# Kernel tuning notes

Hardware: AMD Instinct MI355X
Metric: run time of the kernel (lower is better)

## Reference

```python
import jax, jax.numpy as jnp
import numpy as np

TAGSET = 50
START_TAG = 48
END_TAG = 49
SEQ_LEN = 512
BATCH = 64
HIDDEN = 512


def setup_inputs() -> dict:
    key = jax.random.key(0)
    k1, k2, k3, k4 = jax.random.split(key, 4)
    feats = jax.random.normal(k1, (SEQ_LEN, BATCH, HIDDEN), dtype=jnp.float32)
    W = jax.random.normal(k2, (TAGSET * TAGSET, HIDDEN), dtype=jnp.float32) * (1.0 / np.sqrt(HIDDEN))
    b = jax.random.normal(k3, (TAGSET * TAGSET,), dtype=jnp.float32) * 0.01
    target = jax.random.randint(k4, (SEQ_LEN, BATCH, 1), 0, TAGSET * TAGSET, dtype=jnp.int64)
    mask = jnp.ones((SEQ_LEN, BATCH), dtype=bool)
    return {"feats": feats, "W": W, "b": b, "target": target, "mask": mask}


def reference(feats, W, b, target, mask):
    S, B, H = feats.shape
    T = TAGSET
    # hidden2tag: Linear(H -> T*T), then view (S, B, T_from, T_to)
    scores = jnp.einsum('sbh,kh->sbk', feats, W) + b  # (S, B, T*T)
    scores4 = scores.reshape(S, B, T, T)

    # gold-path energy: gather flattened (from,to) index per position, mask, sum
    tg_energy = jnp.take_along_axis(scores, target, axis=2)[..., 0]  # (S, B)
    tg_sum = jnp.sum(jnp.where(mask, tg_energy, jnp.zeros((), scores.dtype)))

    # forward algorithm (log-sum-exp semiring scan over time)
    partition0 = scores4[0, :, START_TAG, :]  # (B, T)

    def step(partition, xs):
        cur, m = xs  # cur: (B, T_from, T_to), m: (B,)
        new = jax.nn.logsumexp(cur + partition[:, :, None], axis=1)  # (B, T)
        partition = jnp.where(m[:, None], new, partition)
        return partition, None

    partition, _ = jax.lax.scan(step, partition0, (scores4[1:], mask[1:]))
    loss = (jnp.sum(partition[:, END_TAG]) - tg_sum) / B
    return loss
```

## Files before the change

### kernel.cpp

```cpp
#include <hip/hip_runtime.h>
#include <math.h>


#define KK    2500
#define KPAD  2560
#define NROW  32768
#define MTS   72
#define MTS2  80
#define ARS   144
#define LN2   0.69314718055994530942f
#define LOG2E 1.44269504088896340736f

typedef __attribute__((ext_vector_type(8))) short short8;
typedef __attribute__((ext_vector_type(8))) unsigned short ushort8;
typedef __attribute__((ext_vector_type(4))) float f32x4;
typedef __attribute__((ext_vector_type(4))) int int4v;
typedef __attribute__((ext_vector_type(8))) int int8v;
typedef __attribute__((ext_vector_type(2))) unsigned int uint2v;

__device__ __forceinline__ unsigned short f2bf(float f){
  unsigned int u = __builtin_bit_cast(unsigned int, f);
  u += 0x7fffu + ((u >> 16) & 1u);
  return (unsigned short)(u >> 16);
}
__device__ __forceinline__ float bf2f(unsigned short h){
  return __builtin_bit_cast(float, ((unsigned int)h) << 16);
}
__device__ __forceinline__ unsigned int pk_fp8x4(float a0, float a1, float a2, float a3){
  unsigned int p = __builtin_amdgcn_cvt_pk_fp8_f32(a0, a1, 0, false);
  p = __builtin_amdgcn_cvt_pk_fp8_f32(a2, a3, p, true);
  return p;
}

__global__ __launch_bounds__(256) void prep_kernel(const float* __restrict__ feats,
                                                   const float* __restrict__ W,
                                                   const float* __restrict__ bias_in,
                                                   unsigned char* __restrict__ A8,
                                                   unsigned char* __restrict__ W8,
                                                   float* __restrict__ bias_pad,
                                                   float* __restrict__ out){
  const int bid = blockIdx.x, t = threadIdx.x;
  if (bid < 8192){
    const int i = (bid * 256 + t) << 3;
    f32x4 a = *(const f32x4*)(feats + i);
    f32x4 b = *(const f32x4*)(feats + i + 4);
    uint2v o;
    o[0] = pk_fp8x4(a[0], a[1], a[2], a[3]);
    o[1] = pk_fp8x4(b[0], b[1], b[2], b[3]);
    *(uint2v*)(A8 + i) = o;
  } else if (bid < 8832){
    const int i = ((bid - 8192) * 256 + t) << 3;
    uint2v o = {0u, 0u};
    if (i < 1280000){
      f32x4 a = *(const f32x4*)(W + i);
      f32x4 b = *(const f32x4*)(W + i + 4);
      o[0] = pk_fp8x4(a[0], a[1], a[2], a[3]);
      o[1] = pk_fp8x4(b[0], b[1], b[2], b[3]);
    }
    *(uint2v*)(W8 + i) = o;
  } else {
    const int i = (bid - 8832) * 256 + t;
    if (i < KPAD) bias_pad[i] = (i < KK) ? bias_in[i] : 0.0f;
    if (i == 0) out[0] = 0.0f;
  }
}

__global__ __launch_bounds__(256) void gemm_exp_kernel(
    const unsigned char* __restrict__ A8,
    const unsigned char* __restrict__ W8,
    const float* __restrict__ bias,
    const int* __restrict__ target,
    unsigned short* __restrict__ E,
    float* __restrict__ out)
{
  __shared__ alignas(16) unsigned char smem[2 * 128 * ARS];
  __shared__ int Ts[128];
  __shared__ float r4[4];
  unsigned char* As = smem;
  unsigned char* Bs = smem + 128 * ARS;
  unsigned short* Ep = (unsigned short*)smem;
  const int t = threadIdx.x;
  const int lane = t & 63, w = t >> 6;
  const int f = blockIdx.y * 20 + blockIdx.x;
  const int v = (f & 7) * 640 + (f >> 3);
  const int by = v / 20, bx = v - by * 20;
  const int Rbase = by * 128;
  const int Cbase = bx * 128;
  const int m0 = (w >> 1) * 64, n0 = (w & 1) * 64;
  const int fr = lane & 15;
  const int quad = lane >> 4;
  if (t < 128) Ts[t] = target[Rbase + t];
  const int srow = t >> 3, scol = (t & 7) * 16;

  f32x4 acc[4][4];
  const f32x4 vz = {0.f, 0.f, 0.f, 0.f};
  #pragma unroll
  for (int i = 0; i < 4; i++)
    #pragma unroll
    for (int j = 0; j < 4; j++) acc[i][j] = vz;

  int4v ar[4], br[4];
  #pragma unroll
  for (int q = 0; q < 4; q++){
    const int row = srow + q * 32;
    ar[q] = *(const int4v*)(A8 + (size_t)(Rbase + row) * 512 + scol);
    br[q] = *(const int4v*)(W8 + (size_t)(Cbase + row) * 512 + scol);
  }
  for (int kt = 0; kt < 4; kt++){
    __syncthreads();
    #pragma unroll
    for (int q = 0; q < 4; q++){
      const int row = srow + q * 32;
      *(int4v*)&As[row * ARS + scol] = ar[q];
      *(int4v*)&Bs[row * ARS + scol] = br[q];
    }
    __syncthreads();
    if (kt < 3){
      const int k0 = (kt + 1) * 128;
      #pragma unroll
      for (int q = 0; q < 4; q++){
        const int row = srow + q * 32;
        ar[q] = *(const int4v*)(A8 + (size_t)(Rbase + row) * 512 + k0 + scol);
        br[q] = *(const int4v*)(W8 + (size_t)(Cbase + row) * 512 + k0 + scol);
      }
    }
    int8v af[4], bf[4];
    #pragma unroll
    for (int mf = 0; mf < 4; mf++) af[mf] = *(const int8v*)&As[(m0 + mf * 16 + fr) * ARS + quad * 32];
    #pragma unroll
    for (int nf = 0; nf < 4; nf++) bf[nf] = *(const int8v*)&Bs[(n0 + nf * 16 + fr) * ARS + quad * 32];
    #pragma unroll
    for (int mf = 0; mf < 4; mf++)
      #pragma unroll
      for (int nf = 0; nf < 4; nf++)
        acc[mf][nf] = __builtin_amdgcn_mfma_scale_f32_16x16x128_f8f6f4(
            af[mf], bf[nf], acc[mf][nf], 0, 0, 0, 0x7F, 0, 0x7F);
  }
  __syncthreads();
  float tsum = 0.0f;
  int tgv[4][4];
  #pragma unroll
  for (int mf = 0; mf < 4; mf++)
    #pragma unroll
    for (int r = 0; r < 4; r++) tgv[mf][r] = Ts[m0 + mf * 16 + quad * 4 + r];
  #pragma unroll
  for (int nf = 0; nf < 4; nf++){
    const int col = n0 + nf * 16 + fr;
    const int gc = Cbase + col;
    const float bv = bias[gc];
    #pragma unroll
    for (int mf = 0; mf < 4; mf++){
      const int row0 = m0 + mf * 16 + quad * 4;
      #pragma unroll
      for (int r = 0; r < 4; r++){
        const float sc = acc[mf][nf][r] + bv;
        if (gc == tgv[mf][r]) tsum += sc;
        Ep[(row0 + r) * 128 + col] = f2bf(exp2f(sc * LOG2E - 9.0f));
      }
    }
  }
  for (int off = 32; off; off >>= 1) tsum += __shfl_xor(tsum, off);
  if (lane == 0) r4[w] = tsum;
  __syncthreads();
  {
    #pragma unroll
    for (int i = 0; i < 8; i++){
      const int row = w * 32 + i * 4 + quad;
      int4v vv = *(const int4v*)(Ep + row * 128 + fr * 8);
      *(int4v*)(E + (size_t)(Rbase + row) * KPAD + Cbase + fr * 8) = vv;
    }
  }
  if (t == 0) atomicAdd(out, -(r4[0] + r4[1] + r4[2] + r4[3]) * (1.0f / 64.0f));
}

__global__ __launch_bounds__(256) void chunk_prod_kernel(const unsigned short* __restrict__ E,
                                                         unsigned short* __restrict__ Pc,
                                                         float* __restrict__ lsc){
  const int c = blockIdx.x, b = blockIdx.y;
  const int s0 = 1 + c * 8;
  const int L = (s0 + 8 <= 512) ? 8 : (512 - s0);
  __shared__ alignas(16) unsigned short Pl[64 * MTS];
  __shared__ alignas(16) unsigned short Mt[4096];
  __shared__ float red[4];
  const int t = threadIdx.x;
  const int lane = t & 63, w = t >> 6;
  const int m0 = (w >> 1) * 32, n0 = (w & 1) * 32;
  const int fr = lane & 15, fk = (lane >> 4) * 8;
  const int pj = t >> 2, pr = (t & 3) << 4;
  const int pg0 = ((pr >> 3) ^ (pj & 7)) << 3;
  const int pg1 = (((pr >> 3) | 1) ^ (pj & 7)) << 3;

  for (int i = t; i < 64 * MTS; i += 256) Pl[i] = 0;
  for (int i = 3200 + t; i < 4096; i += 256) Mt[i] = 0;
  __syncthreads();
  {
    const unsigned short* rowp = E + (size_t)((s0 + L - 1) * 64 + b) * KPAD;
    ushort8 x0 = *(const ushort8*)(rowp + t * 8);
    #pragma unroll
    for (int u = 0; u < 8; u++){ int k = t * 8 + u; Pl[(k % 50) * MTS + (k / 50)] = x0[u]; }
    if (t < 57){
      ushort8 x1 = *(const ushort8*)(rowp + (t + 256) * 8);
      #pragma unroll
      for (int u = 0; u < 8; u++){ int k = (t + 256) * 8 + u; if (k < KK) Pl[(k % 50) * MTS + (k / 50)] = x1[u]; }
    }
  }
  int pv[8];
  {
    const unsigned short* rowp = E + (size_t)((s0 + L - 2) * 64 + b) * KPAD;
    if (pj < 50){
      const int* sp = (const int*)(rowp + pj * 50 + pr);
      #pragma unroll
      for (int u = 0; u < 8; u++) pv[u] = sp[u];
    }
  }
  f32x4 acc[2][2];
  const f32x4 vz = {0.f, 0.f, 0.f, 0.f};
  for (int step = 1; step < L; step++){
    if (pj < 50){
      int4v lo, hi;
      lo[0]=pv[0]; lo[1]=pv[1]; lo[2]=pv[2]; lo[3]=pv[3];
      hi[0]=pv[4]; hi[1]=pv[5]; hi[2]=pv[6]; hi[3]=pv[7];
      *(int4v*)&Mt[(pj << 6) + pg0] = lo;
      *(int4v*)&Mt[(pj << 6) + pg1] = hi;
    }
    if (step > 1){
      #pragma unroll
      for (int mf = 0; mf < 2; mf++)
        #pragma unroll
        for (int nf = 0; nf < 2; nf++)
          #pragma unroll
          for (int r = 0; r < 4; r++){
            int mm = m0 + mf * 16 + (lane >> 4) * 4 + r;
            int nn = n0 + nf * 16 + fr;
            Pl[mm * MTS + nn] = (nn < 50) ? f2bf(acc[mf][nf][r]) : (unsigned short)0;
          }
    }
    __syncthreads();
    if (step + 1 < L){
      const unsigned short* rowp = E + (size_t)((s0 + L - 2 - step) * 64 + b) * KPAD;
      if (pj < 50){
        const int* sp = (const int*)(rowp + pj * 50 + pr);
        #pragma unroll
        for (int u = 0; u < 8; u++) pv[u] = sp[u];
      }
    }
    acc[0][0] = vz; acc[0][1] = vz; acc[1][0] = vz; acc[1][1] = vz;
    #pragma unroll
    for (int ks = 0; ks < 2; ks++){
      const int k0 = ks * 32 + fk;
      const int j0 = n0 + fr, j1 = n0 + 16 + fr;
      short8 a0 = *(const short8*)&Pl[(m0 + fr) * MTS + k0];
      short8 a1 = *(const short8*)&Pl[(m0 + 16 + fr) * MTS + k0];
      short8 b0 = *(const short8*)&Mt[(j0 << 6) + ((((k0 >> 3) ^ (j0 & 7))) << 3)];
      short8 b1 = *(const short8*)&Mt[(j1 << 6) + ((((k0 >> 3) ^ (j1 & 7))) << 3)];
      acc[0][0] = __builtin_amdgcn_mfma_f32_16x16x32_bf16(a0, b0, acc[0][0], 0, 0, 0);
      acc[0][1] = __builtin_amdgcn_mfma_f32_16x16x32_bf16(a0, b1, acc[0][1], 0, 0, 0);
      acc[1][0] = __builtin_amdgcn_mfma_f32_16x16x32_bf16(a1, b0, acc[1][0], 0, 0, 0);
      acc[1][1] = __builtin_amdgcn_mfma_f32_16x16x32_bf16(a1, b1, acc[1][1], 0, 0, 0);
    }
    __syncthreads();
  }
  float mx = 0.0f;
  #pragma unroll
  for (int mf = 0; mf < 2; mf++)
    #pragma unroll
    for (int nf = 0; nf < 2; nf++)
      #pragma unroll
      for (int r = 0; r < 4; r++) mx = fmaxf(mx, acc[mf][nf][r]);
  for (int off = 32; off; off >>= 1) mx = fmaxf(mx, __shfl_xor(mx, off));
  if (lane == 0) red[w] = mx;
  __syncthreads();
  float gmax = fmaxf(fmaxf(red[0], red[1]), fmaxf(red[2], red[3]));
  float inv = 1.0f / gmax;
  unsigned short* outp = Pc + (size_t)(b * 64 + c) * 4096;
  #pragma unroll
  for (int mf = 0; mf < 2; mf++)
    #pragma unroll
    for (int nf = 0; nf < 2; nf++)
      #pragma unroll
      for (int r = 0; r < 4; r++){
        int mm = m0 + mf * 16 + (lane >> 4) * 4 + r;
        int nn = n0 + nf * 16 + fr;
        outp[mm * 64 + nn] = (nn < 50) ? f2bf(acc[mf][nf][r] * inv) : (unsigned short)0;
      }
  if (t == 0) lsc[b * 64 + c] = logf(gmax) + (float)L * 9.0f * LN2;
}

__global__ __launch_bounds__(256) void oct_prod_kernel(const unsigned short* __restrict__ In,
                                                       const float* __restrict__ lsin,
                                                       unsigned short* __restrict__ Out,
                                                       float* __restrict__ lsout,
                                                       int ncin, int fan,
                                                       const unsigned short* __restrict__ E,
                                                       float* __restrict__ out, int finish){
  const int jo = blockIdx.x, b = blockIdx.y, ncout = gridDim.x;
  const size_t base = ((size_t)b * ncin + jo * fan) * 4096;
  __shared__ alignas(16) unsigned short Pl[64 * MTS2];
  __shared__ alignas(16) unsigned short Mt[64 * MTS2];
  __shared__ float red[4];
  const int t = threadIdx.x;
  const int lane = t & 63, w = t >> 6;
  const int m0 = (w >> 1) * 32, n0 = (w & 1) * 32;
  const int fr = lane & 15, fk = (lane >> 4) * 8;
  for (int i = t; i < 64 * MTS2; i += 256){ Pl[i] = 0; Mt[i] = 0; }
  __syncthreads();
  {
    const ushort8* src = (const ushort8*)(In + base + (size_t)(finish ? (fan - 1) : 0) * 4096);
    ushort8 x0 = src[t], x1 = src[t + 256];
    const int r0 = t >> 3, nb = (t & 7) * 8;
    #pragma unroll
    for (int i = 0; i < 8; i++) Pl[(nb + i) * MTS2 + r0] = x0[i];
    const int r1 = (t + 256) >> 3;
    #pragma unroll
    for (int i = 0; i < 8; i++) Pl[(nb + i) * MTS2 + r1] = x1[i];
  }
  f32x4 acc[2][2];
  const f32x4 vz = {0.f, 0.f, 0.f, 0.f};
  for (int f = 1; f < fan; f++){
    const int mi = finish ? (fan - 1 - f) : f;
    const ushort8* src = (const ushort8*)(In + base + (size_t)mi * 4096);
    ushort8 x0 = src[t], x1 = src[t + 256];
    *(ushort8*)&Mt[(t >> 3) * MTS2 + (t & 7) * 8] = x0;
    *(ushort8*)&Mt[((t + 256) >> 3) * MTS2 + (t & 7) * 8] = x1;
    if (f > 1){
      #pragma unroll
      for (int mf = 0; mf < 2; mf++)
        #pragma unroll
        for (int nf = 0; nf < 2; nf++)
          #pragma unroll
          for (int r = 0; r < 4; r++){
            int mm = m0 + mf * 16 + (lane >> 4) * 4 + r;
            int nn = n0 + nf * 16 + fr;
            Pl[mm * MTS2 + nn] = f2bf(acc[mf][nf][r]);
          }
    }
    __syncthreads();
    acc[0][0] = vz; acc[0][1] = vz; acc[1][0] = vz; acc[1][1] = vz;
    #pragma unroll
    for (int ks = 0; ks < 2; ks++){
      const int k0 = ks * 32 + fk;
      short8 a0 = *(const short8*)&Pl[(m0 + fr) * MTS2 + k0];
      short8 a1 = *(const short8*)&Pl[(m0 + 16 + fr) * MTS2 + k0];
      short8 b0 = *(const short8*)&Mt[(n0 + fr) * MTS2 + k0];
      short8 b1 = *(const short8*)&Mt[(n0 + 16 + fr) * MTS2 + k0];
      acc[0][0] = __builtin_amdgcn_mfma_f32_16x16x32_bf16(a0, b0, acc[0][0], 0, 0, 0);
      acc[0][1] = __builtin_amdgcn_mfma_f32_16x16x32_bf16(a0, b1, acc[0][1], 0, 0, 0);
      acc[1][0] = __builtin_amdgcn_mfma_f32_16x16x32_bf16(a1, b0, acc[1][0], 0, 0, 0);
      acc[1][1] = __builtin_amdgcn_mfma_f32_16x16x32_bf16(a1, b1, acc[1][1], 0, 0, 0);
    }
    __syncthreads();
  }
  float mx = 0.0f;
  #pragma unroll
  for (int mf = 0; mf < 2; mf++)
    #pragma unroll
    for (int nf = 0; nf < 2; nf++)
      #pragma unroll
      for (int r = 0; r < 4; r++) mx = fmaxf(mx, acc[mf][nf][r]);
  for (int off = 32; off; off >>= 1) mx = fmaxf(mx, __shfl_xor(mx, off));
  if (lane == 0) red[w] = mx;
  __syncthreads();
  float gmax = fmaxf(fmaxf(red[0], red[1]), fmaxf(red[2], red[3]));
  float inv = 1.0f / gmax;
  if (!finish){
    unsigned short* outp = Out + ((size_t)b * ncout + jo) * 4096;
    #pragma unroll
    for (int mf = 0; mf < 2; mf++)
      #pragma unroll
      for (int nf = 0; nf < 2; nf++)
        #pragma unroll
        for (int r = 0; r < 4; r++){
          int mm = m0 + mf * 16 + (lane >> 4) * 4 + r;
          int nn = n0 + nf * 16 + fr;
          outp[mm * 64 + nn] = f2bf(acc[mf][nf][r] * inv);
        }
    if (t == 0){
      const float* lp = lsin + (size_t)b * ncin + jo * fan;
      float s = 0.0f;
      for (int i = 0; i < fan; i++) s += lp[i];
      lsout[(size_t)b * ncout + jo] = s + logf(gmax);
    }
  } else {
    #pragma unroll
    for (int mf = 0; mf < 2; mf++)
      #pragma unroll
      for (int nf = 0; nf < 2; nf++)
        #pragma unroll
        for (int r = 0; r < 4; r++){
          int mm = m0 + mf * 16 + (lane >> 4) * 4 + r;
          int nn = n0 + nf * 16 + fr;
          Pl[mm * MTS2 + nn] = f2bf(acc[mf][nf][r] * inv);
        }
    __syncthreads();
    if (t < 64){
      float p0 = (t < 50) ? bf2f(E[(size_t)b * KPAD + 48 * 50 + t]) : 0.0f;
      float v = p0 * bf2f(Pl[49 * MTS2 + t]);
      for (int off = 32; off; off >>= 1) v += __shfl_xor(v, off);
      if (t == 0){
        const float* lp = lsin + (size_t)b * ncin + jo * fan;
        float s = 0.0f;
        for (int i = 0; i < fan; i++) s += lp[i];
        atomicAdd(out, (logf(v) + 9.0f * LN2 + s + logf(gmax)) * (1.0f / 64.0f));
      }
    }
  }
}

extern "C" void kernel_launch(void* const* d_in, const int* in_sizes, int n_in,
                              void* d_out, int out_size, void* d_ws, size_t ws_size,
                              hipStream_t stream){
  const float* feats  = (const float*)d_in[0];
  const float* W      = (const float*)d_in[1];
  const float* bias   = (const float*)d_in[2];
  const int*   target = (const int*)d_in[3];
  float* out = (float*)d_out;
  char* ws = (char*)d_ws;
  unsigned char*  A8   = (unsigned char*)(ws + 0);
  unsigned char*  W8   = (unsigned char*)(ws + 16777216);
  float*          bpad = (float*)(ws + 18087936);
  unsigned short* E    = (unsigned short*)(ws + 18098176);
  unsigned short* Pc   = (unsigned short*)(ws + 185870336);
  float*          lsc  = (float*)(ws + 219424768);
  unsigned short* T1   = (unsigned short*)(ws + 0);
  float*          ls1  = (float*)(ws + 4194304);

  prep_kernel<<<8842, 256, 0, stream>>>(feats, W, bias, A8, W8, bpad, out);
  gemm_exp_kernel<<<dim3(20, 256), 256, 0, stream>>>(A8, W8, bpad, target, E, out);
  chunk_prod_kernel<<<dim3(64, 64), 256, 0, stream>>>(E, Pc, lsc);
  oct_prod_kernel<<<dim3(8, 64), 256, 0, stream>>>(Pc, lsc, T1, ls1, 64, 8, E, out, 0);
  oct_prod_kernel<<<dim3(1, 64), 256, 0, stream>>>(T1, ls1, T1, ls1, 8, 8, E, out, 1);
}
```

Baseline: 256.1 us.

## Swizzle GEMM LDS tiles and write exp outputs directly to global

Replaces the padded LDS tile layout (144-byte row stride) with an unpadded 128-byte row layout that uses an XOR swizzle, splitting each 32-byte fragment load into two 16-byte reads to avoid bank conflicts. The epilogue no longer stages the bf16 exp tile in LDS before a coalesced copy. Each lane now stores 2-byte values straight to global memory, target values are read from global, and each wave does its own atomic add. This removes two barriers and the LDS staging, but the global stores become scattered 2-byte writes and there are four times as many atomics.

```diff
diff --git a/kernel.cpp b/kernel.cpp
--- a/kernel.cpp
+++ b/kernel.cpp
@@ -7,7 +7,6 @@
 #define NROW  32768
 #define MTS   72
 #define MTS2  80
-#define ARS   144
 #define LN2   0.69314718055994530942f
 #define LOG2E 1.44269504088896340736f
 
@@ -73,12 +72,8 @@
     unsigned short* __restrict__ E,
     float* __restrict__ out)
 {
-  __shared__ alignas(16) unsigned char smem[2 * 128 * ARS];
-  __shared__ int Ts[128];
-  __shared__ float r4[4];
-  unsigned char* As = smem;
-  unsigned char* Bs = smem + 128 * ARS;
-  unsigned short* Ep = (unsigned short*)smem;
+  __shared__ alignas(16) unsigned char As[16384];
+  __shared__ alignas(16) unsigned char Bs[16384];
   const int t = threadIdx.x;
   const int lane = t & 63, w = t >> 6;
   const int f = blockIdx.y * 20 + blockIdx.x;
@@ -89,8 +84,8 @@
   const int m0 = (w >> 1) * 64, n0 = (w & 1) * 64;
   const int fr = lane & 15;
   const int quad = lane >> 4;
-  if (t < 128) Ts[t] = target[Rbase + t];
   const int srow = t >> 3, scol = (t & 7) * 16;
+  const int swg = (((t & 7) ^ (srow & 7)) << 4);
 
   f32x4 acc[4][4];
   const f32x4 vz = {0.f, 0.f, 0.f, 0.f};
@@ -111,8 +106,8 @@
     #pragma unroll
     for (int q = 0; q < 4; q++){
       const int row = srow + q * 32;
-      *(int4v*)&As[row * ARS + scol] = ar[q];
-      *(int4v*)&Bs[row * ARS + scol] = br[q];
+      *(int4v*)&As[(row << 7) + swg] = ar[q];
+      *(int4v*)&Bs[(row << 7) + swg] = br[q];
     }
     __syncthreads();
     if (kt < 3){
@@ -126,9 +121,27 @@
     }
     int8v af[4], bf[4];
     #pragma unroll
-    for (int mf = 0; mf < 4; mf++) af[mf] = *(const int8v*)&As[(m0 + mf * 16 + fr) * ARS + quad * 32];
-    #pragma unroll
-    for (int nf = 0; nf < 4; nf++) bf[nf] = *(const int8v*)&Bs[(n0 + nf * 16 + fr) * ARS + quad * 32];
+    for (int mf = 0; mf < 4; mf++){
+      const int row = m0 + mf * 16 + fr;
+      const int s7 = row & 7;
+      const unsigned char* p = As + (row << 7);
+      int4v lo = *(const int4v*)(p + (((quad * 2    ) ^ s7) << 4));
+      int4v hi = *(const int4v*)(p + (((quad * 2 + 1) ^ s7) << 4));
+      int8v a; a[0]=lo[0]; a[1]=lo[1]; a[2]=lo[2]; a[3]=lo[3];
+               a[4]=hi[0]; a[5]=hi[1]; a[6]=hi[2]; a[7]=hi[3];
+      af[mf] = a;
+    }
+    #pragma unroll
+    for (int nf = 0; nf < 4; nf++){
+      const int row = n0 + nf * 16 + fr;
+      const int s7 = row & 7;
+      const unsigned char* p = Bs + (row << 7);
+      int4v lo = *(const int4v*)(p + (((quad * 2    ) ^ s7) << 4));
+      int4v hi = *(const int4v*)(p + (((quad * 2 + 1) ^ s7) << 4));
+      int8v b; b[0]=lo[0]; b[1]=lo[1]; b[2]=lo[2]; b[3]=lo[3];
+               b[4]=hi[0]; b[5]=hi[1]; b[6]=hi[2]; b[7]=hi[3];
+      bf[nf] = b;
+    }
     #pragma unroll
     for (int mf = 0; mf < 4; mf++)
       #pragma unroll
@@ -136,41 +149,29 @@
         acc[mf][nf] = __builtin_amdgcn_mfma_scale_f32_16x16x128_f8f6f4(
             af[mf], bf[nf], acc[mf][nf], 0, 0, 0, 0x7F, 0, 0x7F);
   }
-  __syncthreads();
   float tsum = 0.0f;
   int tgv[4][4];
   #pragma unroll
   for (int mf = 0; mf < 4; mf++)
     #pragma unroll
-    for (int r = 0; r < 4; r++) tgv[mf][r] = Ts[m0 + mf * 16 + quad * 4 + r];
+    for (int r = 0; r < 4; r++) tgv[mf][r] = target[Rbase + m0 + mf * 16 + quad * 4 + r];
   #pragma unroll
   for (int nf = 0; nf < 4; nf++){
-    const int col = n0 + nf * 16 + fr;
-    const int gc = Cbase + col;
+    const int gc = Cbase + n0 + nf * 16 + fr;
     const float bv = bias[gc];
     #pragma unroll
     for (int mf = 0; mf < 4; mf++){
-      const int row0 = m0 + mf * 16 + quad * 4;
+      const int gm0 = Rbase + m0 + mf * 16 + quad * 4;
       #pragma unroll
       for (int r = 0; r < 4; r++){
         const float sc = acc[mf][nf][r] + bv;
         if (gc == tgv[mf][r]) tsum += sc;
-        Ep[(row0 + r) * 128 + col] = f2bf(exp2f(sc * LOG2E - 9.0f));
+        E[(size_t)(gm0 + r) * KPAD + gc] = f2bf(exp2f(sc * LOG2E - 9.0f));
       }
     }
   }
   for (int off = 32; off; off >>= 1) tsum += __shfl_xor(tsum, off);
-  if (lane == 0) r4[w] = tsum;
-  __syncthreads();
-  {
-    #pragma unroll
-    for (int i = 0; i < 8; i++){
-      const int row = w * 32 + i * 4 + quad;
-      int4v vv = *(const int4v*)(Ep + row * 128 + fr * 8);
-      *(int4v*)(E + (size_t)(Rbase + row) * KPAD + Cbase + fr * 8) = vv;
-    }
-  }
-  if (t == 0) atomicAdd(out, -(r4[0] + r4[1] + r4[2] + r4[3]) * (1.0f / 64.0f));
+  if (lane == 0) atomicAdd(out, -tsum * (1.0f / 64.0f));
 }
 
 __global__ __launch_bounds__(256) void chunk_prod_kernel(const unsigned short* __restrict__ E,
```

After: 436.3 us. 1.7x slower.
